# Kernel tuning notes

Hardware: AMD Instinct MI355X
Metric: run time of the kernel (lower is better)

Reference implementation:

```python
import jax, jax.numpy as jnp
import numpy as np

EPS = 1e-5


def setup_inputs() -> dict:
    key = jax.random.key(0)
    kx, ky = jax.random.split(key)
    n, d, num_classes = 32768, 128, 64
    x = jax.random.normal(kx, (n, d), dtype=jnp.float32)
    y = jax.random.randint(ky, (n,), 0, num_classes, dtype=jnp.int64)
    return {"x": x, "y": y, "num_classes": num_classes}


def reference(x, y, num_classes):
    n, d = x.shape
    m = n // 2
    x_support, x_target = x[:m], x[m:]
    y_support, y_target = y[:m], y[m:]

    # prototypes: scatter-add instead of one-hot multiply+sum (same math)
    class_counts = jax.ops.segment_sum(
        jnp.ones((m,), x.dtype), y_support, num_segments=num_classes)
    class_counts = class_counts + (class_counts < 0.01).astype(x.dtype)
    prototypes = jax.ops.segment_sum(
        x_support, y_support, num_segments=num_classes) / class_counts[:, None]

    # broadcast distance with the module's custom 'square'
    diff = x_target[:, None, :] - prototypes[None, :, :]  # (m, C, d)
    sq = jnp.sign(diff) * jnp.exp(2.0 * jnp.log(jnp.abs(diff + EPS)))
    distance = -jnp.mean(sq, axis=2)  # (m, C) logits

    # cross entropy (mean over batch)
    logp = jax.nn.log_softmax(distance, axis=1)
    loss = -jnp.take_along_axis(logp, y_target[:, None], axis=1).mean()
    return loss
```

## Files before the change

kernel.cpp:

```cpp
#include <hip/hip_runtime.h>

#define M_HALF 16384
#define D 128
#define C 64

#define KP_BLOCKS 512
#define KC_BLOCKS 256
#define KC_ROWS 64

__global__ __launch_bounds__(256) void kp_proto(
    const float* __restrict__ x, const int* __restrict__ y,
    float* __restrict__ pTg,
    float* __restrict__ out)
{
    __shared__ float red[4][16];
    __shared__ int   credw[4];
    const int tid  = threadIdx.x;
    const int lane = tid & 63;
    const int wid  = tid >> 6;
    const int blk  = blockIdx.x;
    const int myc  = blk & 63;
    const int kq8  = blk >> 6;

    if (blk == 0 && tid == 0) out[0] = 0.f;

    float acc[16];
    #pragma unroll
    for (int j = 0; j < 16; ++j) acc[j] = 0.f;
    int cnt = 0;

    const float* xb = x + kq8 * 16;
    const int4* y4 = (const int4*)y;

    #pragma unroll
    for (int half = 0; half < 2; ++half) {
        int4 yv[8];
        #pragma unroll
        for (int i = 0; i < 8; ++i)
            yv[i] = y4[(half * 8 + i) * 256 + tid];
        #pragma unroll
        for (int i = 0; i < 8; ++i) {
            const int r0 = ((half * 8 + i) * 256 + tid) * 4;
            const int4 v = yv[i];
            #pragma unroll
            for (int s = 0; s < 4; ++s) {
                const int yl = (s == 0) ? v.x : (s == 1) ? v.y : (s == 2) ? v.z : v.w;
                if (yl == myc) {
                    ++cnt;
                    const float4* xr = (const float4*)(xb + (size_t)(r0 + s) * D);
                    #pragma unroll
                    for (int j4 = 0; j4 < 4; ++j4) {
                        const float4 vv = xr[j4];
                        acc[j4*4+0] += vv.x; acc[j4*4+1] += vv.y;
                        acc[j4*4+2] += vv.z; acc[j4*4+3] += vv.w;
                    }
                }
            }
        }
    }

    #pragma unroll
    for (int off = 32; off; off >>= 1) {
        #pragma unroll
        for (int j = 0; j < 16; ++j) acc[j] += __shfl_xor(acc[j], off);
        cnt += __shfl_xor(cnt, off);
    }
    if (lane == 0) {
        #pragma unroll
        for (int j = 0; j < 16; ++j) red[wid][j] = acc[j];
        credw[wid] = cnt;
    }
    __syncthreads();
    if (tid < 16) {
        float tot = red[0][tid] + red[1][tid] + red[2][tid] + red[3][tid];
        float c = (float)(credw[0] + credw[1] + credw[2] + credw[3]);
        if (c < 0.5f) c = 1.f;
        tot /= c;
        const int k = kq8 * 16 + tid;
        pTg[((k >> 2) * 64 + (myc & 3) * 16 + (myc >> 2)) * 4 + (k & 3)] = tot;
    }
}

__global__ __launch_bounds__(256) void kc_dist_loss(
    const float* __restrict__ x, const int* __restrict__ y,
    const float4* __restrict__ pTg4,
    float* __restrict__ out)
{
    __shared__ float4 pT4[32 * 64];
    __shared__ float  wsum[4];
    const int tid = threadIdx.x;

    for (int o = tid; o < 32 * 64; o += 256) pT4[o] = pTg4[o];
    __syncthreads();

    const int lane = tid & 63;
    const int wid  = tid >> 6;
    const int cg   = lane & 15;
    const int rg   = lane >> 4;
    const int rbase = wid * 16 + rg * 4;
    const int row0 = M_HALF + blockIdx.x * KC_ROWS;

    const float4* xrow[4];
    #pragma unroll
    for (int r = 0; r < 4; ++r)
        xrow[r] = (const float4*)(x + (size_t)(row0 + rbase + r) * D);

    float acc[4][4];
    #pragma unroll
    for (int r = 0; r < 4; ++r)
        #pragma unroll
        for (int cc = 0; cc < 4; ++cc) acc[r][cc] = 0.f;

    float4 xv[4], xvn[4];
    #pragma unroll
    for (int r = 0; r < 4; ++r) xv[r] = xrow[r][0];

    #pragma unroll 4
    for (int k4 = 0; k4 < 32; ++k4) {
        if (k4 < 31) {
            #pragma unroll
            for (int r = 0; r < 4; ++r) xvn[r] = xrow[r][k4 + 1];
        }
        float4 pv[4];
        #pragma unroll
        for (int cc = 0; cc < 4; ++cc) pv[cc] = pT4[k4 * 64 + cc * 16 + cg];
        #pragma unroll
        for (int r = 0; r < 4; ++r) {
            #pragma unroll
            for (int cc = 0; cc < 4; ++cc) {
                float d;
                d = xv[r].x - pv[cc].x; acc[r][cc] = fmaf(d, fabsf(d), acc[r][cc]);
                d = xv[r].y - pv[cc].y; acc[r][cc] = fmaf(d, fabsf(d), acc[r][cc]);
                d = xv[r].z - pv[cc].z; acc[r][cc] = fmaf(d, fabsf(d), acc[r][cc]);
                d = xv[r].w - pv[cc].w; acc[r][cc] = fmaf(d, fabsf(d), acc[r][cc]);
            }
        }
        #pragma unroll
        for (int r = 0; r < 4; ++r) xv[r] = xvn[r];
    }

    const float ninv_d = -1.f / (float)D;
    float lsum = 0.f;
    #pragma unroll
    for (int r = 0; r < 4; ++r) {
        float dv0 = acc[r][0] * ninv_d, dv1 = acc[r][1] * ninv_d;
        float dv2 = acc[r][2] * ninv_d, dv3 = acc[r][3] * ninv_d;
        float mx = fmaxf(fmaxf(dv0, dv1), fmaxf(dv2, dv3));
        #pragma unroll
        for (int off = 8; off; off >>= 1) mx = fmaxf(mx, __shfl_xor(mx, off));
        float se = __expf(dv0 - mx) + __expf(dv1 - mx) +
                   __expf(dv2 - mx) + __expf(dv3 - mx);
        #pragma unroll
        for (int off = 8; off; off >>= 1) se += __shfl_xor(se, off);
        const float lse = mx + __logf(se);

        const int yt  = y[row0 + rbase + r];
        const int cct = yt & 3, cgt = yt >> 2;
        const float v01 = (cct & 1) ? dv1 : dv0;
        const float v23 = (cct & 1) ? dv3 : dv2;
        const float val = (cct & 2) ? v23 : v01;
        const float dy  = __shfl(val, (lane & 48) | cgt);
        lsum += lse - dy;
    }

    lsum += __shfl_xor(lsum, 16);
    lsum += __shfl_xor(lsum, 32);

    if (lane == 0) wsum[wid] = lsum;
    __syncthreads();
    if (tid == 0) {
        const float tot = (wsum[0] + wsum[1] + wsum[2] + wsum[3]) * (1.f / (float)M_HALF);
        atomicAdd(out, tot);
    }
}

extern "C" void kernel_launch(void* const* d_in, const int* in_sizes, int n_in,
                              void* d_out, int out_size, void* d_ws, size_t ws_size,
                              hipStream_t stream) {
    const float* x = (const float*)d_in[0];
    const int*   y = (const int*)d_in[1];
    float* out = (float*)d_out;

    float* pTg = (float*)d_ws;

    kp_proto<<<KP_BLOCKS, 256, 0, stream>>>(x, y, pTg, out);
    kc_dist_loss<<<KC_BLOCKS, 256, 0, stream>>>(x, y, (const float4*)pTg, out);
}
```

Baseline: 36.26 us.

## Fuse prototype and distance kernels into one cooperative launch with grid sync

Merges the prototype-computation and distance/loss kernels into a single cooperative kernel separated by a grid-wide barrier, which removes the second kernel launch and its inter-kernel gap. To fit the 256-block grid, each prototype block now accumulates 32 feature columns instead of 16, so it does twice as much per-row work. If the cooperative launch fails, the code falls back to two separate launches. The price is the grid.sync cost and fewer, heavier phase-A blocks that each rescan all the labels.

After: 70.12 us. 1.93x slower.

```diff
diff --git a/kernel.cpp b/kernel.cpp
--- a/kernel.cpp
+++ b/kernel.cpp
@@ -1,37 +1,34 @@
 #include <hip/hip_runtime.h>
+#include <hip/hip_cooperative_groups.h>
+
+namespace cg = cooperative_groups;
 
 #define M_HALF 16384
 #define D 128
 #define C 64
-
-#define KP_BLOCKS 512
-#define KC_BLOCKS 256
+#define NBLK 256
 #define KC_ROWS 64
 
-__global__ __launch_bounds__(256) void kp_proto(
-    const float* __restrict__ x, const int* __restrict__ y,
-    float* __restrict__ pTg,
-    float* __restrict__ out)
-{
-    __shared__ float red[4][16];
+__device__ __forceinline__ void phase_a(
+    const float* __restrict__ x, const int* __restrict__ y,
+    float* __restrict__ pTg, float* __restrict__ out, int blk, int tid)
+{
+    __shared__ float redA[4][32];
     __shared__ int   credw[4];
-    const int tid  = threadIdx.x;
     const int lane = tid & 63;
     const int wid  = tid >> 6;
-    const int blk  = blockIdx.x;
     const int myc  = blk & 63;
-    const int kq8  = blk >> 6;
+    const int kq   = blk >> 6;
 
     if (blk == 0 && tid == 0) out[0] = 0.f;
 
-    float acc[16];
-    #pragma unroll
-    for (int j = 0; j < 16; ++j) acc[j] = 0.f;
+    float acc[32];
+    #pragma unroll
+    for (int j = 0; j < 32; ++j) acc[j] = 0.f;
     int cnt = 0;
 
-    const float* xb = x + kq8 * 16;
+    const float* xb = x + kq * 32;
     const int4* y4 = (const int4*)y;
-
     #pragma unroll
     for (int half = 0; half < 2; ++half) {
         int4 yv[8];
@@ -49,7 +46,7 @@
                     ++cnt;
                     const float4* xr = (const float4*)(xb + (size_t)(r0 + s) * D);
                     #pragma unroll
-                    for (int j4 = 0; j4 < 4; ++j4) {
+                    for (int j4 = 0; j4 < 8; ++j4) {
                         const float4 vv = xr[j4];
                         acc[j4*4+0] += vv.x; acc[j4*4+1] += vv.y;
                         acc[j4*4+2] += vv.z; acc[j4*4+3] += vv.w;
@@ -62,43 +59,41 @@
     #pragma unroll
     for (int off = 32; off; off >>= 1) {
         #pragma unroll
-        for (int j = 0; j < 16; ++j) acc[j] += __shfl_xor(acc[j], off);
+        for (int j = 0; j < 32; ++j) acc[j] += __shfl_xor(acc[j], off);
         cnt += __shfl_xor(cnt, off);
     }
     if (lane == 0) {
         #pragma unroll
-        for (int j = 0; j < 16; ++j) red[wid][j] = acc[j];
+        for (int j = 0; j < 32; ++j) redA[wid][j] = acc[j];
         credw[wid] = cnt;
     }
     __syncthreads();
-    if (tid < 16) {
-        float tot = red[0][tid] + red[1][tid] + red[2][tid] + red[3][tid];
+    if (tid < 32) {
+        float tot = redA[0][tid] + redA[1][tid] + redA[2][tid] + redA[3][tid];
         float c = (float)(credw[0] + credw[1] + credw[2] + credw[3]);
         if (c < 0.5f) c = 1.f;
         tot /= c;
-        const int k = kq8 * 16 + tid;
+        const int k = kq * 32 + tid;
         pTg[((k >> 2) * 64 + (myc & 3) * 16 + (myc >> 2)) * 4 + (k & 3)] = tot;
     }
 }
 
-__global__ __launch_bounds__(256) void kc_dist_loss(
-    const float* __restrict__ x, const int* __restrict__ y,
-    const float4* __restrict__ pTg4,
-    float* __restrict__ out)
+__device__ __forceinline__ void phase_c(
+    const float* __restrict__ x, const int* __restrict__ y,
+    const float4* __restrict__ pTg4, float* __restrict__ out, int blk, int tid)
 {
     __shared__ float4 pT4[32 * 64];
     __shared__ float  wsum[4];
-    const int tid = threadIdx.x;
 
     for (int o = tid; o < 32 * 64; o += 256) pT4[o] = pTg4[o];
     __syncthreads();
 
     const int lane = tid & 63;
     const int wid  = tid >> 6;
-    const int cg   = lane & 15;
+    const int cg_  = lane & 15;
     const int rg   = lane >> 4;
     const int rbase = wid * 16 + rg * 4;
-    const int row0 = M_HALF + blockIdx.x * KC_ROWS;
+    const int row0 = M_HALF + blk * KC_ROWS;
 
     const float4* xrow[4];
     #pragma unroll
@@ -123,7 +118,7 @@
         }
         float4 pv[4];
         #pragma unroll
-        for (int cc = 0; cc < 4; ++cc) pv[cc] = pT4[k4 * 64 + cc * 16 + cg];
+        for (int cc = 0; cc < 4; ++cc) pv[cc] = pT4[k4 * 64 + cc * 16 + cg_];
         #pragma unroll
         for (int r = 0; r < 4; ++r) {
             #pragma unroll
@@ -174,15 +169,43 @@
     }
 }
 
+__global__ __launch_bounds__(256) void fused_coop(
+    const float* __restrict__ x, const int* __restrict__ y,
+    float* __restrict__ pTg, float* __restrict__ out)
+{
+    cg::grid_group grid = cg::this_grid();
+    phase_a(x, y, pTg, out, blockIdx.x, threadIdx.x);
+    grid.sync();
+    phase_c(x, y, (const float4*)pTg, out, blockIdx.x, threadIdx.x);
+}
+
+__global__ __launch_bounds__(256) void kp_fb(
+    const float* __restrict__ x, const int* __restrict__ y,
+    float* __restrict__ pTg, float* __restrict__ out)
+{
+    phase_a(x, y, pTg, out, blockIdx.x, threadIdx.x);
+}
+
+__global__ __launch_bounds__(256) void kc_fb(
+    const float* __restrict__ x, const int* __restrict__ y,
+    const float4* __restrict__ pTg4, float* __restrict__ out)
+{
+    phase_c(x, y, pTg4, out, blockIdx.x, threadIdx.x);
+}
+
 extern "C" void kernel_launch(void* const* d_in, const int* in_sizes, int n_in,
                               void* d_out, int out_size, void* d_ws, size_t ws_size,
                               hipStream_t stream) {
     const float* x = (const float*)d_in[0];
     const int*   y = (const int*)d_in[1];
     float* out = (float*)d_out;
-
     float* pTg = (float*)d_ws;
 
-    kp_proto<<<KP_BLOCKS, 256, 0, stream>>>(x, y, pTg, out);
-    kc_dist_loss<<<KC_BLOCKS, 256, 0, stream>>>(x, y, (const float4*)pTg, out);
-}
+    void* args[] = { (void*)&x, (void*)&y, (void*)&pTg, (void*)&out };
+    hipError_t err = hipLaunchCooperativeKernel(
+        (const void*)fused_coop, dim3(NBLK), dim3(256), args, 0, stream);
+    if (err != hipSuccess) {
+        kp_fb<<<NBLK, 256, 0, stream>>>(x, y, pTg, out);
+        kc_fb<<<NBLK, 256, 0, stream>>>(x, y, (const float4*)pTg, out);
+    }
+}
```

## Split distance reduction dimension across two wave groups in kc_dist_loss

Applied to the files above, without the earlier changes.

Doubles the block size of the distance/loss kernel to 512 threads. Each half of the waves accumulates half of the D dimension, and the second half's partial sums are merged through shared memory before the softmax and loss. This halves the serial inner-loop length per thread and doubles the wave count, aiming for more latency hiding on a grid of only 256 blocks. The cost is an extra 16KB of LDS, an extra barrier, and half the waves sitting idle during the epilogue.

After: 35.09 us. 3.2% less time.

```diff
diff --git a/kernel.cpp b/kernel.cpp
--- a/kernel.cpp
+++ b/kernel.cpp
@@ -81,23 +81,27 @@
     }
 }
 
-__global__ __launch_bounds__(256) void kc_dist_loss(
+__global__ __launch_bounds__(512) void kc_dist_loss(
     const float* __restrict__ x, const int* __restrict__ y,
     const float4* __restrict__ pTg4,
     float* __restrict__ out)
 {
     __shared__ float4 pT4[32 * 64];
+    __shared__ float  comb[4][16][64];
     __shared__ float  wsum[4];
     const int tid = threadIdx.x;
 
-    for (int o = tid; o < 32 * 64; o += 256) pT4[o] = pTg4[o];
+    for (int o = tid; o < 32 * 64; o += 512) pT4[o] = pTg4[o];
     __syncthreads();
 
     const int lane = tid & 63;
     const int wid  = tid >> 6;
+    const int wrow = wid & 3;
+    const int khal = wid >> 2;
+    const int k4lo = khal * 16;
     const int cg   = lane & 15;
     const int rg   = lane >> 4;
-    const int rbase = wid * 16 + rg * 4;
+    const int rbase = wrow * 16 + rg * 4;
     const int row0 = M_HALF + blockIdx.x * KC_ROWS;
 
     const float4* xrow[4];
@@ -113,11 +117,12 @@
 
     float4 xv[4], xvn[4];
     #pragma unroll
-    for (int r = 0; r < 4; ++r) xv[r] = xrow[r][0];
+    for (int r = 0; r < 4; ++r) xv[r] = xrow[r][k4lo];
 
     #pragma unroll 4
-    for (int k4 = 0; k4 < 32; ++k4) {
-        if (k4 < 31) {
+    for (int k4i = 0; k4i < 16; ++k4i) {
+        const int k4 = k4lo + k4i;
+        if (k4i < 15) {
             #pragma unroll
             for (int r = 0; r < 4; ++r) xvn[r] = xrow[r][k4 + 1];
         }
@@ -139,34 +144,51 @@
         for (int r = 0; r < 4; ++r) xv[r] = xvn[r];
     }
 
-    const float ninv_d = -1.f / (float)D;
-    float lsum = 0.f;
-    #pragma unroll
-    for (int r = 0; r < 4; ++r) {
-        float dv0 = acc[r][0] * ninv_d, dv1 = acc[r][1] * ninv_d;
-        float dv2 = acc[r][2] * ninv_d, dv3 = acc[r][3] * ninv_d;
-        float mx = fmaxf(fmaxf(dv0, dv1), fmaxf(dv2, dv3));
-        #pragma unroll
-        for (int off = 8; off; off >>= 1) mx = fmaxf(mx, __shfl_xor(mx, off));
-        float se = __expf(dv0 - mx) + __expf(dv1 - mx) +
-                   __expf(dv2 - mx) + __expf(dv3 - mx);
-        #pragma unroll
-        for (int off = 8; off; off >>= 1) se += __shfl_xor(se, off);
-        const float lse = mx + __logf(se);
-
-        const int yt  = y[row0 + rbase + r];
-        const int cct = yt & 3, cgt = yt >> 2;
-        const float v01 = (cct & 1) ? dv1 : dv0;
-        const float v23 = (cct & 1) ? dv3 : dv2;
-        const float val = (cct & 2) ? v23 : v01;
-        const float dy  = __shfl(val, (lane & 48) | cgt);
-        lsum += lse - dy;
-    }
-
-    lsum += __shfl_xor(lsum, 16);
-    lsum += __shfl_xor(lsum, 32);
-
-    if (lane == 0) wsum[wid] = lsum;
+    if (khal == 1) {
+        #pragma unroll
+        for (int r = 0; r < 4; ++r)
+            #pragma unroll
+            for (int cc = 0; cc < 4; ++cc)
+                comb[wrow][r * 4 + cc][lane] = acc[r][cc];
+    }
+    __syncthreads();
+
+    if (khal == 0) {
+        #pragma unroll
+        for (int r = 0; r < 4; ++r)
+            #pragma unroll
+            for (int cc = 0; cc < 4; ++cc)
+                acc[r][cc] += comb[wrow][r * 4 + cc][lane];
+
+        const float ninv_d = -1.f / (float)D;
+        float lsum = 0.f;
+        #pragma unroll
+        for (int r = 0; r < 4; ++r) {
+            float dv0 = acc[r][0] * ninv_d, dv1 = acc[r][1] * ninv_d;
+            float dv2 = acc[r][2] * ninv_d, dv3 = acc[r][3] * ninv_d;
+            float mx = fmaxf(fmaxf(dv0, dv1), fmaxf(dv2, dv3));
+            #pragma unroll
+            for (int off = 8; off; off >>= 1) mx = fmaxf(mx, __shfl_xor(mx, off));
+            float se = __expf(dv0 - mx) + __expf(dv1 - mx) +
+                       __expf(dv2 - mx) + __expf(dv3 - mx);
+            #pragma unroll
+            for (int off = 8; off; off >>= 1) se += __shfl_xor(se, off);
+            const float lse = mx + __logf(se);
+
+            const int yt  = y[row0 + rbase + r];
+            const int cct = yt & 3, cgt = yt >> 2;
+            const float v01 = (cct & 1) ? dv1 : dv0;
+            const float v23 = (cct & 1) ? dv3 : dv2;
+            const float val = (cct & 2) ? v23 : v01;
+            const float dy  = __shfl(val, (lane & 48) | cgt);
+            lsum += lse - dy;
+        }
+
+        lsum += __shfl_xor(lsum, 16);
+        lsum += __shfl_xor(lsum, 32);
+
+        if (lane == 0) wsum[wrow] = lsum;
+    }
     __syncthreads();
     if (tid == 0) {
         const float tot = (wsum[0] + wsum[1] + wsum[2] + wsum[3]) * (1.f / (float)M_HALF);
@@ -184,5 +206,5 @@
     float* pTg = (float*)d_ws;
 
     kp_proto<<<KP_BLOCKS, 256, 0, stream>>>(x, y, pTg, out);
-    kc_dist_loss<<<KC_BLOCKS, 256, 0, stream>>>(x, y, (const float4*)pTg, out);
+    kc_dist_loss<<<KC_BLOCKS, 512, 0, stream>>>(x, y, (const float4*)pTg, out);
 }
```
